# Optimization experiments

Hardware: AMD Instinct MI355X
Metric: run time of the kernel (lower is better)

## Reference

```python
import jax, jax.numpy as jnp
import numpy as np
import math

B, S = 8, 2048
N_HIDDEN_RNN = 512
D_MODEL = 1024
NUM_HEADS = 16
N_OUTPUT = 1024
SCALE = math.sqrt(D_MODEL // NUM_HEADS)  # head_dim used only for scaling


def setup_inputs() -> dict:
    key = jax.random.key(0)
    ks = jax.random.split(key, 11)
    def lin(k, fan_in, fan_out):
        bound = 1.0 / math.sqrt(fan_in)
        kw, kb = jax.random.split(k)
        W = jax.random.uniform(kw, (fan_out, fan_in), jnp.float32, -bound, bound)
        b = jax.random.uniform(kb, (fan_out,), jnp.float32, -bound, bound)
        return W, b
    Wq, bq = lin(ks[0], N_HIDDEN_RNN, D_MODEL)
    Wk, bk = lin(ks[1], D_MODEL, D_MODEL)
    Wv, bv = lin(ks[2], D_MODEL, D_MODEL)
    Wo, bo = lin(ks[3], D_MODEL, N_OUTPUT)
    return {
        "query": jax.random.normal(ks[4], (B, S, N_HIDDEN_RNN), jnp.float32),
        "key": jax.random.normal(ks[5], (B, S, D_MODEL), jnp.float32),
        "value": jax.random.normal(ks[6], (B, S, D_MODEL), jnp.float32),
        "Wq": Wq, "bq": bq, "Wk": Wk, "bk": bk,
        "Wv": Wv, "bv": bv, "Wo": Wo, "bo": bo,
    }


def reference(query, key, value, Wq, bq, Wk, bk, Wv, bv, Wo, bo):
    # Projections
    q = query @ Wq.T + bq      # [B, S, d_model]
    k = key @ Wk.T + bk        # [B, S, d_model]
    v = value @ Wv.T + bv      # [B, S, d_model]
    # Original code transposes to [B, d_model, S] (feature-axis attention).
    # scores[b, i, j] = sum_s q[b, s, i] * k[b, s, j] / scale -> [B, d, d]
    scores = jnp.einsum('bsi,bsj->bij', q, k) / SCALE
    probs = jax.nn.softmax(scores, axis=-1)   # softmax over feature axis j
    # out[b, s, i] = sum_j probs[b, i, j] * v[b, s, j]
    attn_out = jnp.einsum('bij,bsj->bsi', probs, v)  # [B, S, d_model]
    return attn_out @ Wo.T + bo  # [B, S, n_output]
```

## Files before the change

kernel.cpp:

```cpp
#include <hip/hip_runtime.h>
#include <hip/hip_bf16.h>
#include <stdint.h>

typedef __bf16 b16x8 __attribute__((ext_vector_type(8)));
typedef float  f32x4 __attribute__((ext_vector_type(4)));

__device__ __forceinline__ unsigned short f2bf(float f) {
    uint32_t u = __float_as_uint(f);
    u += 0x7fffu + ((u >> 16) & 1u);
    return (unsigned short)(u >> 16);
}
__device__ __forceinline__ float bf2f(unsigned short s) {
    return __uint_as_float(((uint32_t)s) << 16);
}

__device__ __forceinline__ void gld16(const unsigned short* g, unsigned short* l) {
    __builtin_amdgcn_global_load_lds(
        (const __attribute__((address_space(1))) void*)g,
        (__attribute__((address_space(3))) void*)l, 16, 0, 0);
}

__device__ __forceinline__ void cvt_chunk(const void* src, unsigned short* dst,
                                          long off, int fl) {
    if (fl) {
        const float4* s = (const float4*)src + 2 * off;
        float4 a = s[0], b = s[1];
        uint4 o;
        o.x = f2bf(a.x) | ((uint32_t)f2bf(a.y) << 16);
        o.y = f2bf(a.z) | ((uint32_t)f2bf(a.w) << 16);
        o.z = f2bf(b.x) | ((uint32_t)f2bf(b.y) << 16);
        o.w = f2bf(b.z) | ((uint32_t)f2bf(b.w) << 16);
        ((uint4*)dst)[off] = o;
    } else {
        ((uint4*)dst)[off] = ((const uint4*)src)[off];
    }
}

__global__ __launch_bounds__(256) void k_prep(
    const void* __restrict__ q_in, const void* __restrict__ k_in,
    const void* __restrict__ v_in,
    const void* Wq, const void* bq, const void* Wk, const void* bk,
    const void* Wv, const void* bv, const void* Wo, const void* bo,
    unsigned short* __restrict__ wqb, unsigned short* __restrict__ wkb,
    unsigned short* __restrict__ wvb, unsigned short* __restrict__ wob,
    float* __restrict__ bias4,
    unsigned short* __restrict__ kb, unsigned short* __restrict__ qb,
    unsigned short* __restrict__ vb, int* __restrict__ flag)
{
    float m = 0.f;
    const unsigned short* qraw = (const unsigned short*)q_in;
    for (int i = threadIdx.x; i < 4096; i += 256) {
        float f = fabsf(bf2f(qraw[i]));
        if (!(f < 1e30f)) f = 1e30f;
        m = fmaxf(m, f);
    }
#pragma unroll
    for (int o = 32; o > 0; o >>= 1) m = fmaxf(m, __shfl_xor(m, o));
    __shared__ float red[4];
    if ((threadIdx.x & 63) == 0) red[threadIdx.x >> 6] = m;
    __syncthreads();
    m = fmaxf(fmaxf(red[0], red[1]), fmaxf(red[2], red[3]));
    const int fl = (m > 1e6f) ? 1 : 0;
    if (blockIdx.x == 0 && threadIdx.x == 0) flag[0] = fl;

    if (blockIdx.x < 16) {
        int i = blockIdx.x * 256 + threadIdx.x;
        int which = i >> 10, idx = i & 1023;
        const void* src = (which == 0) ? bq : (which == 1) ? bk : (which == 2) ? bv : bo;
        bias4[i] = fl ? ((const float*)src)[idx] : bf2f(((const unsigned short*)src)[idx]);
    }

    const long NW = 65536L + 3 * 131072L;
    for (long c = blockIdx.x * 256L + threadIdx.x; c < NW; c += (long)gridDim.x * 256L) {
        if (c < 65536)       cvt_chunk(Wq, wqb, c, fl);
        else if (c < 196608) cvt_chunk(Wk, wkb, c - 65536, fl);
        else if (c < 327680) cvt_chunk(Wv, wvb, c - 196608, fl);
        else                 cvt_chunk(Wo, wob, c - 327680, fl);
    }

    const long KN8 = 2097152, QN8 = 1048576, VN8 = 2097152;
    const long TOT = KN8 + QN8 + VN8;
    for (long c = blockIdx.x * 256L + threadIdx.x; c < TOT; c += (long)gridDim.x * 256L) {
        if (c < KN8)            cvt_chunk(k_in, kb, c, fl);
        else if (c < KN8 + QN8) cvt_chunk(q_in, qb, c - KN8, fl);
        else                    cvt_chunk(v_in, vb, c - KN8 - QN8, fl);
    }
}

__device__ __forceinline__ void gemm256(
    const unsigned short* __restrict__ Ab, const unsigned short* __restrict__ Bb,
    const float* __restrict__ bias, void* __restrict__ Cv,
    int N, int K, int ldA, int ldB, int Mb, int am0, long zC, int bn,
    float scale, int mode, int fl, unsigned short* lds)
{
    const int tid  = threadIdx.x;
    const int lane = tid & 63;
    const int wave = tid >> 6;
    const int wm = (wave >> 2) * 128;
    const int wn = (wave & 3) * 64;

    f32x4 acc[8][4];
    const f32x4 zero = {0.f, 0.f, 0.f, 0.f};
#pragma unroll
    for (int i = 0; i < 8; ++i)
#pragma unroll
        for (int j = 0; j < 4; ++j) acc[i][j] = zero;

    auto stage = [&](int kt, int cb) {
        unsigned short* LA = lds + (size_t)cb * 32768;
        unsigned short* LB = LA + 16384;
#pragma unroll
        for (int j = 0; j < 4; ++j) {
            const int d = j * 512 + tid;
            const int row = d >> 3;
            const int klo = (d & 7) ^ (row & 7);
            gld16(Ab + (long)(am0 + row) * ldA + kt * 64 + klo * 8, LA + (size_t)d * 8);
            gld16(Bb + (long)(bn + row) * ldB + kt * 64 + klo * 8, LB + (size_t)d * 8);
        }
    };
    auto ctile = [&](int cb) {
        const unsigned short* LA = lds + (size_t)cb * 32768;
        const unsigned short* LB = LA + 16384;
        b16x8 bfr[4][2];
#pragma unroll
        for (int p = 0; p < 4; ++p) {
            if (p == 0) {
#pragma unroll
                for (int j = 0; j < 4; ++j)
#pragma unroll
                    for (int s = 0; s < 2; ++s) {
                        const int r = wn + j * 16 + (lane & 15);
                        const int kl = s * 4 + (lane >> 4);
                        bfr[j][s] = *(const b16x8*)(LB + ((size_t)r * 8 + (kl ^ (r & 7))) * 8);
                    }
            }
            b16x8 a[2][2];
#pragma unroll
            for (int q = 0; q < 2; ++q)
#pragma unroll
                for (int s = 0; s < 2; ++s) {
                    const int r = wm + (2 * p + q) * 16 + (lane & 15);
                    const int kl = s * 4 + (lane >> 4);
                    a[q][s] = *(const b16x8*)(LA + ((size_t)r * 8 + (kl ^ (r & 7))) * 8);
                }
#pragma unroll
            for (int q = 0; q < 2; ++q)
#pragma unroll
                for (int s = 0; s < 2; ++s)
#pragma unroll
                    for (int j = 0; j < 4; ++j)
                        acc[2 * p + q][j] = __builtin_amdgcn_mfma_f32_16x16x32_bf16(
                            a[q][s], bfr[j][s], acc[2 * p + q][j], 0, 0, 0);
        }
    };

    const int NT = K >> 6;
    stage(0, 0);
    __syncthreads();
    int cur = 0;
    for (int kt = 0; kt < NT - 1; ++kt) {
        stage(kt + 1, cur ^ 1);
        ctile(cur);
        __syncthreads();
        cur ^= 1;
    }
    ctile(cur);

#pragma unroll
    for (int i = 0; i < 8; ++i)
#pragma unroll
        for (int j = 0; j < 4; ++j) {
            const int rloc = am0 + wm + i * 16 + (lane >> 4) * 4;
            const int n    = bn + wn + j * 16 + (lane & 15);
            const float bv = (mode != 2 && bias != nullptr) ? bias[n] : 0.f;
            if (mode == 0) {
                unsigned short* C = (unsigned short*)Cv;
#pragma unroll
                for (int r = 0; r < 4; ++r)
                    C[zC + (long)(rloc + r) * N + n] = f2bf(acc[i][j][r] * scale + bv);
            } else if (mode == 1) {
                unsigned short* C = (unsigned short*)Cv;
                uint32_t p0 = f2bf(acc[i][j][0] * scale + bv) |
                              ((uint32_t)f2bf(acc[i][j][1] * scale + bv) << 16);
                uint32_t p1 = f2bf(acc[i][j][2] * scale + bv) |
                              ((uint32_t)f2bf(acc[i][j][3] * scale + bv) << 16);
                uint2 val; val.x = p0; val.y = p1;
                *(uint2*)(C + zC + (long)n * Mb + rloc) = val;
            } else if (mode == 2) {
                float* C = (float*)Cv;
#pragma unroll
                for (int r = 0; r < 4; ++r)
                    C[zC + (long)(rloc + r) * N + n] = acc[i][j][r] * scale;
            } else {
                if (fl) {
                    float* C = (float*)Cv;
#pragma unroll
                    for (int r = 0; r < 4; ++r)
                        C[zC + (long)(rloc + r) * N + n] = acc[i][j][r] * scale + bv;
                } else {
                    unsigned short* C = (unsigned short*)Cv;
#pragma unroll
                    for (int r = 0; r < 4; ++r)
                        C[zC + (long)(rloc + r) * N + n] = f2bf(acc[i][j][r] * scale + bv);
                }
            }
        }
}

__global__ __launch_bounds__(512, 2) void k_proj3(
    const unsigned short* __restrict__ kb, const unsigned short* __restrict__ qb,
    const unsigned short* __restrict__ vb,
    const unsigned short* __restrict__ wkb, const unsigned short* __restrict__ wqb,
    const unsigned short* __restrict__ wvb,
    const float* __restrict__ bias4,
    unsigned short* __restrict__ Kt, unsigned short* __restrict__ Qt,
    unsigned short* __restrict__ Vp)
{
    extern __shared__ unsigned short lds_raw[];
    const int nwg = gridDim.x * gridDim.y;
    const int bid = blockIdx.y * gridDim.x + blockIdx.x;
    const int vbk = (bid & 7) * (nwg >> 3) + (bid >> 3);
    const int sec = vbk >> 8;
    const int wi  = vbk & 255;
    const int bn  = (wi & 3) * 256;
    const int bm  = (wi >> 2) * 256;
    if (sec == 0) {
        const int batch = bm >> 11, am0 = bm & 2047;
        gemm256(kb + (long)batch * 2048 * 1024, wkb, bias4 + 1024, Kt,
                1024, 1024, 1024, 1024, 2048, am0, (long)batch * 1024 * 2048, bn,
                1.f, 1, 0, lds_raw);
    } else if (sec == 1) {
        const int batch = bm >> 11, am0 = bm & 2047;
        gemm256(qb + (long)batch * 2048 * 512, wqb, bias4, Qt,
                1024, 512, 512, 512, 2048, am0, (long)batch * 1024 * 2048, bn,
                1.f, 1, 0, lds_raw);
    } else {
        gemm256(vb, wvb, bias4 + 2 * 1024, Vp,
                1024, 1024, 1024, 1024, 16384, bm, 0, bn,
                1.f, 0, 0, lds_raw);
    }
}

__global__ __launch_bounds__(512, 2) void k_attn(
    const unsigned short* __restrict__ Vp, const unsigned short* __restrict__ P,
    unsigned short* __restrict__ attn)
{
    extern __shared__ unsigned short lds_raw[];
    const int nwg = gridDim.x * gridDim.y;
    const int bid = blockIdx.y * gridDim.x + blockIdx.x;
    const int vbk = (bid & 7) * (nwg >> 3) + (bid >> 3);
    const int bn  = (vbk & 3) * 256;
    const int bm  = (vbk >> 2) * 256;
    const int batch = bm >> 11, am0 = bm & 2047;
    gemm256(Vp + (long)batch * 2048 * 1024, P + (long)batch * 1024 * 2048,
            nullptr, attn, 1024, 1024, 1024, 2048, 2048, am0,
            (long)batch * 2048 * 1024, bn, 1.f, 0, 0, lds_raw);
}

__global__ __launch_bounds__(512, 2) void k_out(
    const unsigned short* __restrict__ attn, const unsigned short* __restrict__ wob,
    const float* __restrict__ bias4, void* __restrict__ Cv,
    const int* __restrict__ flagp)
{
    extern __shared__ unsigned short lds_raw[];
    const int nwg = gridDim.x * gridDim.y;
    const int bid = blockIdx.y * gridDim.x + blockIdx.x;
    const int vbk = (bid & 7) * (nwg >> 3) + (bid >> 3);
    const int bn  = (vbk & 3) * 256;
    const int bm  = (vbk >> 2) * 256;
    gemm256(attn, wob, bias4 + 3 * 1024, Cv, 1024, 1024, 1024, 1024,
            16384, bm, 0, bn, 1.f, 3, flagp[0], lds_raw);
}

__global__ __launch_bounds__(512, 4) void k_scores(
    const unsigned short* __restrict__ Qt, const unsigned short* __restrict__ Kt,
    float* __restrict__ S)
{
    extern __shared__ unsigned short lds_raw[];
    const int tid  = threadIdx.x;
    const int lane = tid & 63;
    const int wave = tid >> 6;
    const int nwg = gridDim.x * gridDim.y;
    const int bid = blockIdx.y * gridDim.x + blockIdx.x;
    const int vbk = (bid & 7) * (nwg >> 3) + (bid >> 3);
    const int bn  = (vbk & 3) * 256;
    const int bm  = (vbk >> 2) * 128;
    const int batch = bm >> 10, am0 = bm & 1023;
    const unsigned short* Ab = Qt + (long)batch * 1024 * 2048;
    const unsigned short* Bb = Kt + (long)batch * 1024 * 2048;
    const long zC = (long)batch * 1024 * 1024;
    const int wm = (wave >> 2) * 64;
    const int wn = (wave & 3) * 64;

    f32x4 acc[4][4];
    const f32x4 zero = {0.f, 0.f, 0.f, 0.f};
#pragma unroll
    for (int i = 0; i < 4; ++i)
#pragma unroll
        for (int j = 0; j < 4; ++j) acc[i][j] = zero;

    auto stage = [&](int kt, int cb) {
        unsigned short* Lb = lds_raw + (size_t)cb * 12288;
        {
            const int c = tid, row = c >> 2;
            const int klo = (c & 3) ^ ((row >> 1) & 3);
            gld16(Ab + (long)(am0 + row) * 2048 + kt * 32 + klo * 8, Lb + (size_t)c * 8);
        }
#pragma unroll
        for (int j = 0; j < 2; ++j) {
            const int c = j * 512 + tid, row = c >> 2;
            const int klo = (c & 3) ^ ((row >> 1) & 3);
            gld16(Bb + (long)(bn + row) * 2048 + kt * 32 + klo * 8, Lb + 4096 + (size_t)c * 8);
        }
    };
    auto ctile = [&](int cb) {
        const unsigned short* LA = lds_raw + (size_t)cb * 12288;
        const unsigned short* LB = LA + 4096;
        const int kl = lane >> 4;
        b16x8 af[4], bf[4];
#pragma unroll
        for (int j = 0; j < 4; ++j) {
            const int r = wn + j * 16 + (lane & 15);
            bf[j] = *(const b16x8*)(LB + ((size_t)r * 4 + (kl ^ ((r >> 1) & 3))) * 8);
        }
#pragma unroll
        for (int i = 0; i < 4; ++i) {
            const int r = wm + i * 16 + (lane & 15);
            af[i] = *(const b16x8*)(LA + ((size_t)r * 4 + (kl ^ ((r >> 1) & 3))) * 8);
        }
#pragma unroll
        for (int i = 0; i < 4; ++i)
#pragma unroll
            for (int j = 0; j < 4; ++j)
                acc[i][j] = __builtin_amdgcn_mfma_f32_16x16x32_bf16(af[i], bf[j], acc[i][j], 0, 0, 0);
    };

    const int NT = 2048 >> 5;
    stage(0, 0);
    __syncthreads();
    int cur = 0;
    for (int kt = 0; kt < NT - 1; ++kt) {
        stage(kt + 1, cur ^ 1);
        ctile(cur);
        __syncthreads();
        cur ^= 1;
    }
    ctile(cur);

#pragma unroll
    for (int i = 0; i < 4; ++i)
#pragma unroll
        for (int j = 0; j < 4; ++j) {
            const int rloc = am0 + wm + i * 16 + (lane >> 4) * 4;
            const int n    = bn + wn + j * 16 + (lane & 15);
#pragma unroll
            for (int r = 0; r < 4; ++r)
                S[zC + (long)(rloc + r) * 1024 + n] = acc[i][j][r] * 0.125f;
        }
}

__global__ __launch_bounds__(256) void k_softmax(float* __restrict__ S) {
    const long row = blockIdx.x;
    float* s = S + row * 1024;
    unsigned short* p = (unsigned short*)s;
    const int tid = threadIdx.x;
    float4 v = ((const float4*)s)[tid];
    float m = fmaxf(fmaxf(v.x, v.y), fmaxf(v.z, v.w));
#pragma unroll
    for (int o = 32; o > 0; o >>= 1) m = fmaxf(m, __shfl_xor(m, o));
    __shared__ float sm[4], ss[4];
    if ((tid & 63) == 0) sm[tid >> 6] = m;
    __syncthreads();
    m = fmaxf(fmaxf(sm[0], sm[1]), fmaxf(sm[2], sm[3]));
    float e0 = __expf(v.x - m), e1 = __expf(v.y - m);
    float e2 = __expf(v.z - m), e3 = __expf(v.w - m);
    float sum = e0 + e1 + e2 + e3;
#pragma unroll
    for (int o = 32; o > 0; o >>= 1) sum += __shfl_xor(sum, o);
    if ((tid & 63) == 0) ss[tid >> 6] = sum;
    __syncthreads();
    float inv = 1.f / (ss[0] + ss[1] + ss[2] + ss[3]);
    uint32_t w0 = f2bf(e0 * inv) | ((uint32_t)f2bf(e1 * inv) << 16);
    uint32_t w1 = f2bf(e2 * inv) | ((uint32_t)f2bf(e3 * inv) << 16);
    uint2 val; val.x = w0; val.y = w1;
    *(uint2*)(p + tid * 4) = val;
}

extern "C" void kernel_launch(void* const* d_in, const int* in_sizes, int n_in,
                              void* d_out, int out_size, void* d_ws, size_t ws_size,
                              hipStream_t stream) {
    (void)in_sizes; (void)n_in; (void)out_size; (void)ws_size;
    const void* q_in = d_in[0];
    const void* k_in = d_in[1];
    const void* v_in = d_in[2];
    const void* Wq   = d_in[3];
    const void* bq   = d_in[4];
    const void* Wk   = d_in[5];
    const void* bk   = d_in[6];
    const void* Wv   = d_in[7];
    const void* bv   = d_in[8];
    const void* Wo   = d_in[9];
    const void* bo   = d_in[10];

    const size_t MB = 1u << 20;
    const size_t LDS_BIG = 131072, LDS_S = 49152;
    hipFuncSetAttribute((const void*)k_proj3,  hipFuncAttributeMaxDynamicSharedMemorySize, (int)LDS_BIG);
    hipFuncSetAttribute((const void*)k_attn,   hipFuncAttributeMaxDynamicSharedMemorySize, (int)LDS_BIG);
    hipFuncSetAttribute((const void*)k_out,    hipFuncAttributeMaxDynamicSharedMemorySize, (int)LDS_BIG);
    hipFuncSetAttribute((const void*)k_scores, hipFuncAttributeMaxDynamicSharedMemorySize, (int)LDS_S);

    char* ws = (char*)d_ws;
    int*            flag = (int*)ws;
    unsigned short* R1   = (unsigned short*)(ws + 1 * MB);
    unsigned short* R2   = (unsigned short*)(ws + 33 * MB);
    char*           R3   = ws + 65 * MB;
    unsigned short* kb = R1;
    unsigned short* vb = R2, *Vp = R2, *attn = R2;
    float*          scores = (float*)R1;
    unsigned short* P      = R1;
    unsigned short* wqb = (unsigned short*)R3;
    unsigned short* wkb = (unsigned short*)(R3 + 1 * MB);
    unsigned short* wvb = (unsigned short*)(R3 + 3 * MB);
    unsigned short* wob = (unsigned short*)(R3 + 5 * MB);
    float*          bias4 = (float*)(R3 + 7 * MB);
    unsigned short* qb  = (unsigned short*)(R3 + 8 * MB);
    unsigned short* Kt = (unsigned short*)d_out;
    unsigned short* Qt = (unsigned short*)((char*)d_out + 32 * MB);

    dim3 blk(256), blk5(512);
    k_prep<<<dim3(2048), blk, 0, stream>>>(
        q_in, k_in, v_in, Wq, bq, Wk, bk, Wv, bv, Wo, bo,
        wqb, wkb, wvb, wob, bias4, kb, qb, vb, flag);
    k_proj3<<<dim3(4, 192), blk5, LDS_BIG, stream>>>(
        kb, qb, vb, wkb, wqb, wvb, bias4, Kt, Qt, Vp);
    k_scores<<<dim3(4, 64), blk5, LDS_S, stream>>>(Qt, Kt, scores);
    k_softmax<<<dim3(8192), blk, 0, stream>>>(scores);
    k_attn<<<dim3(4, 64), blk5, LDS_BIG, stream>>>(Vp, P, attn);
    k_out<<<dim3(4, 64), blk5, LDS_BIG, stream>>>(attn, wob, bias4, d_out, flag);
}
```

Measured before the change: 281.2 us.

## Switch GEMM mainloop to 4-stage K=32 LDS pipeline with explicit vmcnt waits

```diff
diff --git a/kernel.cpp b/kernel.cpp
--- a/kernel.cpp
+++ b/kernel.cpp
@@ -96,7 +96,7 @@
     const int tid  = threadIdx.x;
     const int lane = tid & 63;
     const int wave = tid >> 6;
-    const int wm = (wave >> 2) * 128;
+    const int g  = wave >> 2;
     const int wn = (wave & 3) * 64;
 
     f32x4 acc[8][4];
@@ -106,71 +106,61 @@
 #pragma unroll
         for (int j = 0; j < 4; ++j) acc[i][j] = zero;
 
-    auto stage = [&](int kt, int cb) {
-        unsigned short* LA = lds + (size_t)cb * 32768;
-        unsigned short* LB = LA + 16384;
+    auto stageD = [&](int t) {
+        unsigned short* S = lds + (size_t)(t & 3) * 16384;
+#pragma unroll
+        for (int j = 0; j < 2; ++j) {
+            const int c = j * 512 + tid;
+            const int row = c >> 2;
+            const int klo = (c & 3) ^ ((row >> 1) & 3);
+            gld16(Ab + (long)(am0 + row) * ldA + t * 32 + klo * 8, S + (size_t)c * 8);
+            gld16(Bb + (long)(bn + row) * ldB + t * 32 + klo * 8, S + 8192 + (size_t)c * 8);
+        }
+    };
+
+    const int NT = K >> 5;
+    stageD(0); stageD(1); stageD(2);
+
+    const int kl = lane >> 4;
+    for (int t = 0; t < NT; ++t) {
+        if (t + 3 < NT) stageD(t + 3);
+        if (t + 3 < NT)      asm volatile("s_waitcnt vmcnt(12)" ::: "memory");
+        else if (t + 2 < NT) asm volatile("s_waitcnt vmcnt(8)"  ::: "memory");
+        else if (t + 1 < NT) asm volatile("s_waitcnt vmcnt(4)"  ::: "memory");
+        else                 asm volatile("s_waitcnt vmcnt(0)"  ::: "memory");
+        __builtin_amdgcn_sched_barrier(0x0F);
+        __builtin_amdgcn_s_barrier();
+        __builtin_amdgcn_sched_barrier(0x0F);
+        const unsigned short* SA = lds + (size_t)(t & 3) * 16384;
+        const unsigned short* SB = SA + 8192;
+        b16x8 af[8], bf[4];
 #pragma unroll
         for (int j = 0; j < 4; ++j) {
-            const int d = j * 512 + tid;
-            const int row = d >> 3;
-            const int klo = (d & 7) ^ (row & 7);
-            gld16(Ab + (long)(am0 + row) * ldA + kt * 64 + klo * 8, LA + (size_t)d * 8);
-            gld16(Bb + (long)(bn + row) * ldB + kt * 64 + klo * 8, LB + (size_t)d * 8);
-        }
-    };
-    auto ctile = [&](int cb) {
-        const unsigned short* LA = lds + (size_t)cb * 32768;
-        const unsigned short* LB = LA + 16384;
-        b16x8 bfr[4][2];
-#pragma unroll
-        for (int p = 0; p < 4; ++p) {
-            if (p == 0) {
-#pragma unroll
-                for (int j = 0; j < 4; ++j)
-#pragma unroll
-                    for (int s = 0; s < 2; ++s) {
-                        const int r = wn + j * 16 + (lane & 15);
-                        const int kl = s * 4 + (lane >> 4);
-                        bfr[j][s] = *(const b16x8*)(LB + ((size_t)r * 8 + (kl ^ (r & 7))) * 8);
-                    }
-            }
-            b16x8 a[2][2];
-#pragma unroll
-            for (int q = 0; q < 2; ++q)
-#pragma unroll
-                for (int s = 0; s < 2; ++s) {
-                    const int r = wm + (2 * p + q) * 16 + (lane & 15);
-                    const int kl = s * 4 + (lane >> 4);
-                    a[q][s] = *(const b16x8*)(LA + ((size_t)r * 8 + (kl ^ (r & 7))) * 8);
-                }
-#pragma unroll
-            for (int q = 0; q < 2; ++q)
-#pragma unroll
-                for (int s = 0; s < 2; ++s)
-#pragma unroll
-                    for (int j = 0; j < 4; ++j)
-                        acc[2 * p + q][j] = __builtin_amdgcn_mfma_f32_16x16x32_bf16(
-                            a[q][s], bfr[j][s], acc[2 * p + q][j], 0, 0, 0);
-        }
-    };
-
-    const int NT = K >> 6;
-    stage(0, 0);
-    __syncthreads();
-    int cur = 0;
-    for (int kt = 0; kt < NT - 1; ++kt) {
-        stage(kt + 1, cur ^ 1);
-        ctile(cur);
-        __syncthreads();
-        cur ^= 1;
-    }
-    ctile(cur);
+            const int r = wn + j * 16 + (lane & 15);
+            bf[j] = *(const b16x8*)(SB + ((size_t)r * 4 + (kl ^ ((r >> 1) & 3))) * 8);
+        }
+#pragma unroll
+        for (int i = 0; i < 8; ++i) {
+            const int r = g * 128 + i * 16 + (lane & 15);
+            af[i] = *(const b16x8*)(SA + ((size_t)r * 4 + (kl ^ ((r >> 1) & 3))) * 8);
+        }
+        __builtin_amdgcn_s_setprio(1);
+#pragma unroll
+        for (int i = 0; i < 8; ++i)
+#pragma unroll
+            for (int j = 0; j < 4; ++j)
+                acc[i][j] = __builtin_amdgcn_mfma_f32_16x16x32_bf16(af[i], bf[j], acc[i][j], 0, 0, 0);
+        __builtin_amdgcn_s_setprio(0);
+        __builtin_amdgcn_sched_barrier(0x0F);
+        __builtin_amdgcn_s_barrier();
+        __builtin_amdgcn_sched_barrier(0x0F);
+    }
 
 #pragma unroll
     for (int i = 0; i < 8; ++i)
 #pragma unroll
         for (int j = 0; j < 4; ++j) {
-            const int rloc = am0 + wm + i * 16 + (lane >> 4) * 4;
+            const int rloc = am0 + g * 128 + i * 16 + (lane >> 4) * 4;
             const int n    = bn + wn + j * 16 + (lane & 15);
             const float bv = (mode != 2 && bias != nullptr) ? bias[n] : 0.f;
             if (mode == 0) {
```

New measurement: 301.2 us. +7.1%, slower.
